# Kernel optimization log

Measured on AMD Instinct MI355X. Metric: run time of the kernel, lower is better.

## Reference

```python
import jax, jax.numpy as jnp
import numpy as np

N = 50000      # current-level nodes
N_NEXT = 2000  # next-level nodes
E = 1600000    # directed edges (before self-loops)
D_IN = 128
D_OUT = 128
LN_EPS = 1e-5


def setup_inputs() -> dict:
    key = jax.random.key(0)
    ks = jax.random.split(key, 12)
    curr_h = jax.random.normal(ks[0], (N, D_IN), dtype=jnp.float32)
    next_h = jax.random.normal(ks[1], (N_NEXT, D_IN), dtype=jnp.float32)
    inc = jax.random.uniform(ks[2], (N, N_NEXT), dtype=jnp.float32)
    src = jax.random.randint(ks[3], (E,), 0, N, dtype=jnp.int64)
    dst = jax.random.randint(ks[4], (E,), 0, N, dtype=jnp.int64)
    s = 1.0 / np.sqrt(D_IN)
    W_conv = jax.random.normal(ks[5], (D_IN, D_OUT), dtype=jnp.float32) * s
    b_conv = jnp.zeros((D_OUT,), dtype=jnp.float32)
    W_fus = jax.random.normal(ks[6], (D_IN, D_OUT), dtype=jnp.float32) * s
    b_fus = jnp.zeros((D_OUT,), dtype=jnp.float32)
    conv_w = jax.random.uniform(ks[7], (D_OUT,), dtype=jnp.float32)
    topDown_w = jax.random.uniform(ks[8], (D_OUT,), dtype=jnp.float32)
    ln_gamma = jnp.ones((D_OUT,), dtype=jnp.float32)
    ln_beta = jnp.zeros((D_OUT,), dtype=jnp.float32)
    return {
        "curr_h": curr_h, "next_h": next_h, "inc": inc,
        "src": src, "dst": dst,
        "W_conv": W_conv, "b_conv": b_conv,
        "W_fus": W_fus, "b_fus": b_fus,
        "conv_w": conv_w, "topDown_w": topDown_w,
        "ln_gamma": ln_gamma, "ln_beta": ln_beta,
    }


def _graph_conv(x, W, b, src_sl, dst_sl, norm_out, norm_in):
    # DGL GraphConv, norm='both': D_out^{-1/2} on src, sum-aggregate, D_in^{-1/2} on dst.
    h = x @ W                               # [N, D_OUT]
    h = h * norm_out[:, None]
    agg = jax.ops.segment_sum(h[src_sl], dst_sl, num_segments=N)  # SpMM
    return agg * norm_in[:, None] + b


def reference(curr_h, next_h, inc, src, dst,
              W_conv, b_conv, W_fus, b_fus,
              conv_w, topDown_w, ln_gamma, ln_beta):
    # dgl.add_self_loop
    loop = jnp.arange(N, dtype=src.dtype)
    src_sl = jnp.concatenate([src, loop])
    dst_sl = jnp.concatenate([dst, loop])
    ones = jnp.ones_like(src_sl, dtype=jnp.float32)
    out_deg = jax.ops.segment_sum(ones, src_sl, num_segments=N)
    in_deg = jax.ops.segment_sum(ones, dst_sl, num_segments=N)
    norm_out = jax.lax.rsqrt(out_deg)  # >=1 due to self-loops
    norm_in = jax.lax.rsqrt(in_deg)

    conv_layer = _graph_conv(curr_h, W_conv, b_conv, src_sl, dst_sl, norm_out, norm_in) * conv_w[None, :]
    fused_in = inc @ next_h  # dense incidence matmul [N, D_IN]
    top_down = _graph_conv(fused_in, W_fus, b_fus, src_sl, dst_sl, norm_out, norm_in) * topDown_w[None, :]

    result = conv_layer + top_down
    # LayerNorm over last dim
    mu = jnp.mean(result, axis=-1, keepdims=True)
    var = jnp.mean((result - mu) ** 2, axis=-1, keepdims=True)
    result = (result - mu) * jax.lax.rsqrt(var + LN_EPS) * ln_gamma + ln_beta
    # dropout p=0.0 (eval) -> identity; activation ReLU
    return jax.nn.relu(result)
```

## Files before the change

kernel.cpp:

```cpp
#include <hip/hip_runtime.h>
#include <hip/hip_bf16.h>

#define N_NODES   50000
#define EDGES     1600000
#define D         128
#define K_INC     2000
#define K_TOT     2128
#define K_PAD     2176
#define KTILES    34
#define LN_EPS    1e-5f

typedef float f32x4 __attribute__((ext_vector_type(4)));
typedef short short8 __attribute__((ext_vector_type(8)));
typedef ushort ushort8v __attribute__((ext_vector_type(8)));

__device__ __forceinline__ ushort f2bf(float x) {
    return __hip_bfloat16_raw(__float2bfloat16(x)).x;
}
__device__ __forceinline__ float bf_lo(uint v) { return __uint_as_float(v << 16); }
__device__ __forceinline__ float bf_hi(uint v) { return __uint_as_float(v & 0xffff0000u); }

#define GLOAD_LDS16(gp, lp) \
    __builtin_amdgcn_global_load_lds((const __attribute__((address_space(1))) void*)(gp), \
                                     (__attribute__((address_space(3))) void*)(lp), 16, 0, 0)

__global__ void probe_kernel(const int* __restrict__ src, int* __restrict__ flag) {
    __shared__ int any_nonzero;
    if (threadIdx.x == 0) any_nonzero = 0;
    __syncthreads();
    int v = src[threadIdx.x * 2 + 1];
    if (v != 0) any_nonzero = 1;
    __syncthreads();
    if (threadIdx.x == 0) flag[0] = any_nonzero ? 0 : 1;
}

__global__ void zero_kernel(int* __restrict__ p, int n) {
    int i = blockIdx.x * 256 + threadIdx.x;
    if (i < n) p[i] = 0;
}

__global__ void deg_kernel(const int* __restrict__ dst, const int* __restrict__ flag,
                           int* __restrict__ in_cnt) {
    int t = blockIdx.x * 256 + threadIdx.x;
    int e0 = t * 2;
    if (e0 >= EDGES) return;
    int d0, d1;
    if (flag[0]) {
        int4 v = *(const int4*)(dst + (size_t)e0 * 2);
        d0 = v.x; d1 = v.z;
    } else {
        int2 v = *(const int2*)(dst + e0);
        d0 = v.x; d1 = v.y;
    }
    atomicAdd(&in_cnt[d0], 1);
    atomicAdd(&in_cnt[d1], 1);
}

__global__ __launch_bounds__(1024) void scan_kernel(const int* __restrict__ cnt,
                                                    int* __restrict__ row_start) {
    __shared__ int buf[1024];
    int t = threadIdx.x;
    const int N = N_NODES;
    int chunk = (N + 1023) / 1024;
    int lo = t * chunk, hi = min(lo + chunk, N);
    int s = 0;
    for (int i = lo; i < hi; ++i) s += cnt[i];
    buf[t] = s;
    __syncthreads();
    for (int off = 1; off < 1024; off <<= 1) {
        int v = (t >= off) ? buf[t - off] : 0;
        __syncthreads();
        buf[t] += v;
        __syncthreads();
    }
    int run = (t > 0) ? buf[t - 1] : 0;
    for (int i = lo; i < hi; ++i) { row_start[i] = run; run += cnt[i]; }
    if (t == 1023) row_start[N] = buf[1023];
}

__global__ void fill_kernel(const int* __restrict__ src, const int* __restrict__ dst,
                            const int* __restrict__ flag,
                            const int* __restrict__ row_start, int* __restrict__ cursor,
                            int* __restrict__ out_deg, int* __restrict__ csr_src) {
    int t = blockIdx.x * 256 + threadIdx.x;
    int e0 = t * 2;
    if (e0 >= EDGES) return;
    int s0, s1, d0, d1;
    if (flag[0]) {
        int4 vs = *(const int4*)(src + (size_t)e0 * 2);
        int4 vd = *(const int4*)(dst + (size_t)e0 * 2);
        s0 = vs.x; s1 = vs.z; d0 = vd.x; d1 = vd.z;
    } else {
        int2 vs = *(const int2*)(src + e0);
        int2 vd = *(const int2*)(dst + e0);
        s0 = vs.x; s1 = vs.y; d0 = vd.x; d1 = vd.y;
    }
    atomicAdd(&out_deg[s0], 1);
    int p0 = atomicAdd(&cursor[d0], 1);
    csr_src[row_start[d0] + p0] = s0;
    atomicAdd(&out_deg[s1], 1);
    int p1 = atomicAdd(&cursor[d1], 1);
    csr_src[row_start[d1] + p1] = s1;
}

#define PKB 16
__global__ __launch_bounds__(128) void p_kernel(
    const float* __restrict__ next_h, const float* __restrict__ W_fus,
    const float* __restrict__ topDown_w, const float* __restrict__ W_conv,
    const float* __restrict__ conv_w, ushort* __restrict__ PbT) {
    int n = threadIdx.x;
    int k0 = blockIdx.x * PKB;
    if (k0 < K_INC) {
        float acc[PKB];
#pragma unroll
        for (int t = 0; t < PKB; ++t) acc[t] = 0.f;
        for (int j = 0; j < D; ++j) {
            float w = W_fus[(size_t)j * D + n];
#pragma unroll
            for (int t = 0; t < PKB; ++t)
                acc[t] += next_h[(size_t)(k0 + t) * D + j] * w;
        }
        float tw = topDown_w[n];
#pragma unroll
        for (int t = 0; t < PKB; ++t)
            PbT[(size_t)n * K_PAD + k0 + t] = f2bf(acc[t] * tw);
    } else if (k0 < K_TOT) {
        float cw = conv_w[n];
#pragma unroll
        for (int t = 0; t < PKB; ++t)
            PbT[(size_t)n * K_PAD + k0 + t] = f2bf(W_conv[(size_t)(k0 + t - K_INC) * D + n] * cw);
    } else {
#pragma unroll
        for (int t = 0; t < PKB; ++t)
            PbT[(size_t)n * K_PAD + k0 + t] = 0;
    }
}

__global__ __launch_bounds__(256, 3) void gemm_kernel(
    const float* __restrict__ inc, const float* __restrict__ curr_h,
    const ushort* __restrict__ PbT, const int* __restrict__ out_deg,
    ushort* __restrict__ Zs) {
    __shared__ __align__(16) ushort As[2][64][72];
    __shared__ __align__(16) ushort Bs[2][128 * 64];
    const int N = N_NODES;
    int tid = threadIdx.x;
    int wave = tid >> 6, lane = tid & 63;
    int wm = wave >> 1, wn = wave & 1;
    int r = lane & 15, q = lane >> 4;
    int rowBase = blockIdx.x * 64;

    f32x4 acc[2][4] = {};
    float4 aReg[2][2];

    auto stage_issue = [&](int kt, int nb) {
        int k0 = kt * 64;
#pragma unroll
        for (int it = 0; it < 2; ++it) {
            int u = tid + it * 256;
            int arow = u >> 3, c8 = u & 7;
            int gk = k0 + c8 * 8;
            int grow = rowBase + arow; if (grow >= N) grow = N - 1;
            if (gk < K_INC) {
                const float4* p4 = (const float4*)(inc + (size_t)grow * K_INC + gk);
                aReg[it][0] = p4[0]; aReg[it][1] = p4[1];
            } else if (gk < K_TOT) {
                const float4* p4 = (const float4*)(curr_h + (size_t)grow * D + (gk - K_INC));
                aReg[it][0] = p4[0]; aReg[it][1] = p4[1];
            } else {
                aReg[it][0] = make_float4(0.f, 0.f, 0.f, 0.f);
                aReg[it][1] = make_float4(0.f, 0.f, 0.f, 0.f);
            }
        }
#pragma unroll
        for (int it = 0; it < 4; ++it) {
            int chunk = tid + it * 256;
            int n = chunk >> 3;
            int c16 = (chunk & 7) << 4;
            int gb = c16 ^ ((n & 7) << 4);
            const char* gp = (const char*)PbT + (size_t)n * (K_PAD * 2) + (size_t)(k0 * 2) + gb;
            char* lp = (char*)(&Bs[nb][0]) + it * 4096 + wave * 1024;
            GLOAD_LDS16(gp, lp);
        }
    };
    auto stage_write = [&](int nb) {
#pragma unroll
        for (int it = 0; it < 2; ++it) {
            int u = tid + it * 256;
            int arow = u >> 3, c8 = u & 7;
            const float* f = (const float*)&aReg[it][0];
            ushort8v hv;
#pragma unroll
            for (int j = 0; j < 8; ++j) hv[j] = f2bf(f[j]);
            *(ushort8v*)&As[nb][arow][c8 * 8] = hv;
        }
    };

    stage_issue(0, 0);
    stage_write(0);
    __syncthreads();

    int cur = 0;
    for (int kt = 0; kt < KTILES; ++kt) {
        int nb = cur ^ 1;
        if (kt + 1 < KTILES) stage_issue(kt + 1, nb);
#pragma unroll
        for (int kk = 0; kk < 2; ++kk) {
            short8 af[2], bfr[4];
#pragma unroll
            for (int mi = 0; mi < 2; ++mi)
                af[mi] = *(const short8*)&As[cur][wm * 32 + mi * 16 + r][kk * 32 + q * 8];
#pragma unroll
            for (int ni = 0; ni < 4; ++ni) {
                int brow = wn * 64 + ni * 16 + r;
                int bcol = (kk * 64 + q * 16) ^ ((r & 7) << 4);
                bfr[ni] = *(const short8*)((const char*)&Bs[cur][0] + brow * 128 + bcol);
            }
#pragma unroll
            for (int mi = 0; mi < 2; ++mi)
#pragma unroll
                for (int ni = 0; ni < 4; ++ni)
                    acc[mi][ni] = __builtin_amdgcn_mfma_f32_16x16x32_bf16(af[mi], bfr[ni], acc[mi][ni], 0, 0, 0);
        }
        if (kt + 1 < KTILES) stage_write(nb);
        __syncthreads();
        cur = nb;
    }

#pragma unroll
    for (int mi = 0; mi < 2; ++mi) {
#pragma unroll
        for (int j = 0; j < 4; ++j) {
            int grow = rowBase + wm * 32 + mi * 16 + q * 4 + j;
            if (grow < N) {
                float no = rsqrtf((float)(out_deg[grow] + 1));
#pragma unroll
                for (int ni = 0; ni < 4; ++ni) {
                    int col = wn * 64 + ni * 16 + r;
                    Zs[(size_t)grow * D + col] = f2bf(acc[mi][ni][j] * no);
                }
            }
        }
    }
}

__global__ __launch_bounds__(256) void agg_ln_kernel(
    const ushort* __restrict__ Zs, const int* __restrict__ row_start,
    const int* __restrict__ csr_src,
    const float* __restrict__ b_conv, const float* __restrict__ b_fus,
    const float* __restrict__ conv_w, const float* __restrict__ topDown_w,
    const float* __restrict__ gamma, const float* __restrict__ beta,
    float* __restrict__ out) {
    int tid = threadIdx.x;
    int wid = tid >> 6, lane = tid & 63;
    int sl = lane & 15;
    int g = lane >> 4;
    int node = blockIdx.x * 16 + wid * 4 + g;
    int c0 = sl * 8;

    float a[8];
    {
        uint4 v = *(const uint4*)(Zs + (size_t)node * D + c0);
        a[0] = bf_lo(v.x); a[1] = bf_hi(v.x);
        a[2] = bf_lo(v.y); a[3] = bf_hi(v.y);
        a[4] = bf_lo(v.z); a[5] = bf_hi(v.z);
        a[6] = bf_lo(v.w); a[7] = bf_hi(v.w);
    }

    int beg = row_start[node], end = row_start[node + 1];
    int deg = end - beg;
    int m = max(deg, __shfl_xor(deg, 16));
    m = max(m, __shfl_xor(m, 32));
    int srcbase = lane & 48;

    for (int base = 0; base < m; base += 16) {
        int idx = 0;
        if (base + sl < deg) idx = csr_src[beg + base + sl];
        int cnt = deg - base;
        if (cnt >= 16) {
#pragma unroll
            for (int i = 0; i < 16; i += 4) {
                int s0 = __shfl(idx, srcbase + i);
                int s1 = __shfl(idx, srcbase + i + 1);
                int s2 = __shfl(idx, srcbase + i + 2);
                int s3 = __shfl(idx, srcbase + i + 3);
                uint4 v0 = *(const uint4*)(Zs + (size_t)s0 * D + c0);
                uint4 v1 = *(const uint4*)(Zs + (size_t)s1 * D + c0);
                uint4 v2 = *(const uint4*)(Zs + (size_t)s2 * D + c0);
                uint4 v3 = *(const uint4*)(Zs + (size_t)s3 * D + c0);
                a[0] += bf_lo(v0.x) + bf_lo(v1.x) + bf_lo(v2.x) + bf_lo(v3.x);
                a[1] += bf_hi(v0.x) + bf_hi(v1.x) + bf_hi(v2.x) + bf_hi(v3.x);
                a[2] += bf_lo(v0.y) + bf_lo(v1.y) + bf_lo(v2.y) + bf_lo(v3.y);
                a[3] += bf_hi(v0.y) + bf_hi(v1.y) + bf_hi(v2.y) + bf_hi(v3.y);
                a[4] += bf_lo(v0.z) + bf_lo(v1.z) + bf_lo(v2.z) + bf_lo(v3.z);
                a[5] += bf_hi(v0.z) + bf_hi(v1.z) + bf_hi(v2.z) + bf_hi(v3.z);
                a[6] += bf_lo(v0.w) + bf_lo(v1.w) + bf_lo(v2.w) + bf_lo(v3.w);
                a[7] += bf_hi(v0.w) + bf_hi(v1.w) + bf_hi(v2.w) + bf_hi(v3.w);
            }
        } else if (cnt > 0) {
            for (int i = 0; i < cnt; ++i) {
                int s0 = __shfl(idx, srcbase + i);
                uint4 v0 = *(const uint4*)(Zs + (size_t)s0 * D + c0);
                a[0] += bf_lo(v0.x); a[1] += bf_hi(v0.x);
                a[2] += bf_lo(v0.y); a[3] += bf_hi(v0.y);
                a[4] += bf_lo(v0.z); a[5] += bf_hi(v0.z);
                a[6] += bf_lo(v0.w); a[7] += bf_hi(v0.w);
            }
        }
    }

    float nin = rsqrtf((float)(deg + 1));
    float4 bc0 = *(const float4*)(b_conv + c0),   bc1 = *(const float4*)(b_conv + c0 + 4);
    float4 cw0 = *(const float4*)(conv_w + c0),   cw1 = *(const float4*)(conv_w + c0 + 4);
    float4 bf0 = *(const float4*)(b_fus + c0),    bf1 = *(const float4*)(b_fus + c0 + 4);
    float4 tw0 = *(const float4*)(topDown_w + c0),tw1 = *(const float4*)(topDown_w + c0 + 4);
    float bias[8] = {
        bc0.x * cw0.x + bf0.x * tw0.x, bc0.y * cw0.y + bf0.y * tw0.y,
        bc0.z * cw0.z + bf0.z * tw0.z, bc0.w * cw0.w + bf0.w * tw0.w,
        bc1.x * cw1.x + bf1.x * tw1.x, bc1.y * cw1.y + bf1.y * tw1.y,
        bc1.z * cw1.z + bf1.z * tw1.z, bc1.w * cw1.w + bf1.w * tw1.w };
    float y[8];
    float s1v = 0.f, s2v = 0.f;
#pragma unroll
    for (int j = 0; j < 8; ++j) {
        y[j] = a[j] * nin + bias[j];
        s1v += y[j]; s2v += y[j] * y[j];
    }
#pragma unroll
    for (int off = 1; off < 16; off <<= 1) {
        s1v += __shfl_xor(s1v, off);
        s2v += __shfl_xor(s2v, off);
    }
    float mu = s1v * (1.f / D);
    float var = s2v * (1.f / D) - mu * mu;
    float rstd = rsqrtf(var + LN_EPS);
    float4 ga0 = *(const float4*)(gamma + c0), ga1 = *(const float4*)(gamma + c0 + 4);
    float4 be0 = *(const float4*)(beta + c0),  be1 = *(const float4*)(beta + c0 + 4);
    float gam[8] = { ga0.x, ga0.y, ga0.z, ga0.w, ga1.x, ga1.y, ga1.z, ga1.w };
    float bet[8] = { be0.x, be0.y, be0.z, be0.w, be1.x, be1.y, be1.z, be1.w };
    float4 o0, o1;
    float r;
    r = (y[0] - mu) * rstd * gam[0] + bet[0]; o0.x = fmaxf(r, 0.f);
    r = (y[1] - mu) * rstd * gam[1] + bet[1]; o0.y = fmaxf(r, 0.f);
    r = (y[2] - mu) * rstd * gam[2] + bet[2]; o0.z = fmaxf(r, 0.f);
    r = (y[3] - mu) * rstd * gam[3] + bet[3]; o0.w = fmaxf(r, 0.f);
    r = (y[4] - mu) * rstd * gam[4] + bet[4]; o1.x = fmaxf(r, 0.f);
    r = (y[5] - mu) * rstd * gam[5] + bet[5]; o1.y = fmaxf(r, 0.f);
    r = (y[6] - mu) * rstd * gam[6] + bet[6]; o1.z = fmaxf(r, 0.f);
    r = (y[7] - mu) * rstd * gam[7] + bet[7]; o1.w = fmaxf(r, 0.f);
    *(float4*)(out + (size_t)node * D + c0) = o0;
    *(float4*)(out + (size_t)node * D + c0 + 4) = o1;
}

extern "C" void kernel_launch(void* const* d_in, const int* in_sizes, int n_in,
                              void* d_out, int out_size, void* d_ws, size_t ws_size,
                              hipStream_t stream) {
    const float* curr_h    = (const float*)d_in[0];
    const float* next_h    = (const float*)d_in[1];
    const float* inc       = (const float*)d_in[2];
    const int*   src       = (const int*)d_in[3];
    const int*   dst       = (const int*)d_in[4];
    const float* W_conv    = (const float*)d_in[5];
    const float* b_conv    = (const float*)d_in[6];
    const float* W_fus     = (const float*)d_in[7];
    const float* b_fus     = (const float*)d_in[8];
    const float* conv_w    = (const float*)d_in[9];
    const float* topDown_w = (const float*)d_in[10];
    const float* ln_gamma  = (const float*)d_in[11];
    const float* ln_beta   = (const float*)d_in[12];

    const int N = N_NODES;
    const int E = EDGES;

    char* p = (char*)d_ws;
    ushort* Zs = (ushort*)p;     p += (size_t)N * D * sizeof(ushort);
    ushort* PbT = (ushort*)p;    p += (size_t)D * K_PAD * 2;
    int* out_deg   = (int*)p;    p += (size_t)N * 4;
    int* in_cnt    = (int*)p;    p += (size_t)N * 4;
    int* cursor    = (int*)p;    p += (size_t)N * 4;
    int* row_start = (int*)p;    p += (size_t)(N + 1) * 4;
    int* idx_flag  = (int*)p;    p += 256;
    int* csr_src   = (int*)p;    p += (size_t)E * 4;

    probe_kernel<<<1, 1024, 0, stream>>>(src, idx_flag);
    zero_kernel<<<(3 * N + 255) / 256, 256, 0, stream>>>(out_deg, 3 * N);
    deg_kernel<<<(E / 2 + 255) / 256, 256, 0, stream>>>(dst, idx_flag, in_cnt);
    scan_kernel<<<1, 1024, 0, stream>>>(in_cnt, row_start);
    fill_kernel<<<(E / 2 + 255) / 256, 256, 0, stream>>>(src, dst, idx_flag, row_start,
                                                         cursor, out_deg, csr_src);
    p_kernel<<<K_PAD / PKB, 128, 0, stream>>>(next_h, W_fus, topDown_w, W_conv, conv_w, PbT);
    gemm_kernel<<<(N + 63) / 64, 256, 0, stream>>>(inc, curr_h, PbT, out_deg, Zs);
    agg_ln_kernel<<<(N + 15) / 16, 256, 0, stream>>>(Zs, row_start, csr_src,
                                                     b_conv, b_fus, conv_w, topDown_w,
                                                     ln_gamma, ln_beta, (float*)d_out);
}
```

Measured before the change: 978.5 us.

## Remap aggregation to one node per wavefront with half-wave edge split

The aggregation+LayerNorm kernel now gives each wavefront a single node instead of four nodes per wave. The two half-waves each gather alternate neighbor rows with 8-byte loads, then combine their partial sums with a cross-half shuffle. This removes idle lanes when degrees differ inside a wave and loads 64 indices per pass instead of 16. The cost is four times as many blocks, smaller per-lane loads, and half the lanes sitting idle during the epilogue and store.

```diff
diff --git a/kernel.cpp b/kernel.cpp
--- a/kernel.cpp
+++ b/kernel.cpp
@@ -250,105 +250,94 @@
     const float* __restrict__ conv_w, const float* __restrict__ topDown_w,
     const float* __restrict__ gamma, const float* __restrict__ beta,
     float* __restrict__ out) {
-    int tid = threadIdx.x;
-    int wid = tid >> 6, lane = tid & 63;
-    int sl = lane & 15;
-    int g = lane >> 4;
-    int node = blockIdx.x * 16 + wid * 4 + g;
-    int c0 = sl * 8;
-
-    float a[8];
-    {
-        uint4 v = *(const uint4*)(Zs + (size_t)node * D + c0);
-        a[0] = bf_lo(v.x); a[1] = bf_hi(v.x);
-        a[2] = bf_lo(v.y); a[3] = bf_hi(v.y);
-        a[4] = bf_lo(v.z); a[5] = bf_hi(v.z);
-        a[6] = bf_lo(v.w); a[7] = bf_hi(v.w);
+    int wid = threadIdx.x >> 6, lane = threadIdx.x & 63;
+    int node = blockIdx.x * 4 + wid;
+    if (node >= N_NODES) return;
+    int half = lane >> 5;
+    int c0 = (lane & 31) * 4;
+
+    float a0 = 0.f, a1 = 0.f, a2 = 0.f, a3 = 0.f;
+    if (!half) {
+        uint2 v = *(const uint2*)(Zs + (size_t)node * D + c0);
+        a0 = bf_lo(v.x); a1 = bf_hi(v.x); a2 = bf_lo(v.y); a3 = bf_hi(v.y);
     }
 
     int beg = row_start[node], end = row_start[node + 1];
     int deg = end - beg;
-    int m = max(deg, __shfl_xor(deg, 16));
-    m = max(m, __shfl_xor(m, 32));
-    int srcbase = lane & 48;
-
-    for (int base = 0; base < m; base += 16) {
+
+    for (int base = 0; base < deg; base += 64) {
+        int rem = deg - base;
+        int cnt = rem < 64 ? rem : 64;
         int idx = 0;
-        if (base + sl < deg) idx = csr_src[beg + base + sl];
-        int cnt = deg - base;
-        if (cnt >= 16) {
-#pragma unroll
-            for (int i = 0; i < 16; i += 4) {
-                int s0 = __shfl(idx, srcbase + i);
-                int s1 = __shfl(idx, srcbase + i + 1);
-                int s2 = __shfl(idx, srcbase + i + 2);
-                int s3 = __shfl(idx, srcbase + i + 3);
-                uint4 v0 = *(const uint4*)(Zs + (size_t)s0 * D + c0);
-                uint4 v1 = *(const uint4*)(Zs + (size_t)s1 * D + c0);
-                uint4 v2 = *(const uint4*)(Zs + (size_t)s2 * D + c0);
-                uint4 v3 = *(const uint4*)(Zs + (size_t)s3 * D + c0);
-                a[0] += bf_lo(v0.x) + bf_lo(v1.x) + bf_lo(v2.x) + bf_lo(v3.x);
-                a[1] += bf_hi(v0.x) + bf_hi(v1.x) + bf_hi(v2.x) + bf_hi(v3.x);
-                a[2] += bf_lo(v0.y) + bf_lo(v1.y) + bf_lo(v2.y) + bf_lo(v3.y);
-                a[3] += bf_hi(v0.y) + bf_hi(v1.y) + bf_hi(v2.y) + bf_hi(v3.y);
-                a[4] += bf_lo(v0.z) + bf_lo(v1.z) + bf_lo(v2.z) + bf_lo(v3.z);
-                a[5] += bf_hi(v0.z) + bf_hi(v1.z) + bf_hi(v2.z) + bf_hi(v3.z);
-                a[6] += bf_lo(v0.w) + bf_lo(v1.w) + bf_lo(v2.w) + bf_lo(v3.w);
-                a[7] += bf_hi(v0.w) + bf_hi(v1.w) + bf_hi(v2.w) + bf_hi(v3.w);
+        if (base + lane < deg) idx = csr_src[beg + base + lane];
+        int np = cnt >> 1;
+        int t = 0;
+        for (; t + 4 <= np; t += 4) {
+            int s0 = __shfl(idx, 2 * t + half);
+            int s1 = __shfl(idx, 2 * t + 2 + half);
+            int s2 = __shfl(idx, 2 * t + 4 + half);
+            int s3 = __shfl(idx, 2 * t + 6 + half);
+            uint2 v0 = *(const uint2*)(Zs + (size_t)s0 * D + c0);
+            uint2 v1 = *(const uint2*)(Zs + (size_t)s1 * D + c0);
+            uint2 v2 = *(const uint2*)(Zs + (size_t)s2 * D + c0);
+            uint2 v3 = *(const uint2*)(Zs + (size_t)s3 * D + c0);
+            a0 += bf_lo(v0.x) + bf_lo(v1.x) + bf_lo(v2.x) + bf_lo(v3.x);
+            a1 += bf_hi(v0.x) + bf_hi(v1.x) + bf_hi(v2.x) + bf_hi(v3.x);
+            a2 += bf_lo(v0.y) + bf_lo(v1.y) + bf_lo(v2.y) + bf_lo(v3.y);
+            a3 += bf_hi(v0.y) + bf_hi(v1.y) + bf_hi(v2.y) + bf_hi(v3.y);
+        }
+        for (; t < np; ++t) {
+            int s0 = __shfl(idx, 2 * t + half);
+            uint2 v0 = *(const uint2*)(Zs + (size_t)s0 * D + c0);
+            a0 += bf_lo(v0.x); a1 += bf_hi(v0.x);
+            a2 += bf_lo(v0.y); a3 += bf_hi(v0.y);
+        }
+        if (cnt & 1) {
+            int s0 = __shfl(idx, cnt - 1);
+            if (!half) {
+                uint2 v0 = *(const uint2*)(Zs + (size_t)s0 * D + c0);
+                a0 += bf_lo(v0.x); a1 += bf_hi(v0.x);
+                a2 += bf_lo(v0.y); a3 += bf_hi(v0.y);
             }
-        } else if (cnt > 0) {
-            for (int i = 0; i < cnt; ++i) {
-                int s0 = __shfl(idx, srcbase + i);
-                uint4 v0 = *(const uint4*)(Zs + (size_t)s0 * D + c0);
-                a[0] += bf_lo(v0.x); a[1] += bf_hi(v0.x);
-                a[2] += bf_lo(v0.y); a[3] += bf_hi(v0.y);
-                a[4] += bf_lo(v0.z); a[5] += bf_hi(v0.z);
-                a[6] += bf_lo(v0.w); a[7] += bf_hi(v0.w);
-            }
-        }
-    }
+        }
+    }
+
+    a0 += __shfl_xor(a0, 32);
+    a1 += __shfl_xor(a1, 32);
+    a2 += __shfl_xor(a2, 32);
+    a3 += __shfl_xor(a3, 32);
 
     float nin = rsqrtf((float)(deg + 1));
-    float4 bc0 = *(const float4*)(b_conv + c0),   bc1 = *(const float4*)(b_conv + c0 + 4);
-    float4 cw0 = *(const float4*)(conv_w + c0),   cw1 = *(const float4*)(conv_w + c0 + 4);
-    float4 bf0 = *(const float4*)(b_fus + c0),    bf1 = *(const float4*)(b_fus + c0 + 4);
-    float4 tw0 = *(const float4*)(topDown_w + c0),tw1 = *(const float4*)(topDown_w + c0 + 4);
-    float bias[8] = {
-        bc0.x * cw0.x + bf0.x * tw0.x, bc0.y * cw0.y + bf0.y * tw0.y,
-        bc0.z * cw0.z + bf0.z * tw0.z, bc0.w * cw0.w + bf0.w * tw0.w,
-        bc1.x * cw1.x + bf1.x * tw1.x, bc1.y * cw1.y + bf1.y * tw1.y,
-        bc1.z * cw1.z + bf1.z * tw1.z, bc1.w * cw1.w + bf1.w * tw1.w };
-    float y[8];
-    float s1v = 0.f, s2v = 0.f;
-#pragma unroll
-    for (int j = 0; j < 8; ++j) {
-        y[j] = a[j] * nin + bias[j];
-        s1v += y[j]; s2v += y[j] * y[j];
-    }
-#pragma unroll
-    for (int off = 1; off < 16; off <<= 1) {
+    float4 bc = *(const float4*)(b_conv + c0);
+    float4 cw = *(const float4*)(conv_w + c0);
+    float4 bfv = *(const float4*)(b_fus + c0);
+    float4 tw = *(const float4*)(topDown_w + c0);
+    float y0 = a0 * nin + bc.x * cw.x + bfv.x * tw.x;
+    float y1 = a1 * nin + bc.y * cw.y + bfv.y * tw.y;
+    float y2 = a2 * nin + bc.z * cw.z + bfv.z * tw.z;
+    float y3 = a3 * nin + bc.w * cw.w + bfv.w * tw.w;
+
+    float s1v = y0 + y1 + y2 + y3;
+    float s2v = y0 * y0 + y1 * y1 + y2 * y2 + y3 * y3;
+#pragma unroll
+    for (int off = 1; off < 32; off <<= 1) {
         s1v += __shfl_xor(s1v, off);
         s2v += __shfl_xor(s2v, off);
     }
     float mu = s1v * (1.f / D);
     float var = s2v * (1.f / D) - mu * mu;
     float rstd = rsqrtf(var + LN_EPS);
-    float4 ga0 = *(const float4*)(gamma + c0), ga1 = *(const float4*)(gamma + c0 + 4);
-    float4 be0 = *(const float4*)(beta + c0),  be1 = *(const float4*)(beta + c0 + 4);
-    float gam[8] = { ga0.x, ga0.y, ga0.z, ga0.w, ga1.x, ga1.y, ga1.z, ga1.w };
-    float bet[8] = { be0.x, be0.y, be0.z, be0.w, be1.x, be1.y, be1.z, be1.w };
-    float4 o0, o1;
-    float r;
-    r = (y[0] - mu) * rstd * gam[0] + bet[0]; o0.x = fmaxf(r, 0.f);
-    r = (y[1] - mu) * rstd * gam[1] + bet[1]; o0.y = fmaxf(r, 0.f);
-    r = (y[2] - mu) * rstd * gam[2] + bet[2]; o0.z = fmaxf(r, 0.f);
-    r = (y[3] - mu) * rstd * gam[3] + bet[3]; o0.w = fmaxf(r, 0.f);
-    r = (y[4] - mu) * rstd * gam[4] + bet[4]; o1.x = fmaxf(r, 0.f);
-    r = (y[5] - mu) * rstd * gam[5] + bet[5]; o1.y = fmaxf(r, 0.f);
-    r = (y[6] - mu) * rstd * gam[6] + bet[6]; o1.z = fmaxf(r, 0.f);
-    r = (y[7] - mu) * rstd * gam[7] + bet[7]; o1.w = fmaxf(r, 0.f);
-    *(float4*)(out + (size_t)node * D + c0) = o0;
-    *(float4*)(out + (size_t)node * D + c0 + 4) = o1;
+    if (!half) {
+        float4 ga = *(const float4*)(gamma + c0);
+        float4 be = *(const float4*)(beta + c0);
+        float4 o;
+        float r;
+        r = (y0 - mu) * rstd * ga.x + be.x; o.x = fmaxf(r, 0.f);
+        r = (y1 - mu) * rstd * ga.y + be.y; o.y = fmaxf(r, 0.f);
+        r = (y2 - mu) * rstd * ga.z + be.z; o.z = fmaxf(r, 0.f);
+        r = (y3 - mu) * rstd * ga.w + be.w; o.w = fmaxf(r, 0.f);
+        *(float4*)(out + (size_t)node * D + c0) = o;
+    }
 }
 
 extern "C" void kernel_launch(void* const* d_in, const int* in_sizes, int n_in,
@@ -389,7 +378,7 @@
                                                          cursor, out_deg, csr_src);
     p_kernel<<<K_PAD / PKB, 128, 0, stream>>>(next_h, W_fus, topDown_w, W_conv, conv_w, PbT);
     gemm_kernel<<<(N + 63) / 64, 256, 0, stream>>>(inc, curr_h, PbT, out_deg, Zs);
-    agg_ln_kernel<<<(N + 15) / 16, 256, 0, stream>>>(Zs, row_start, csr_src,
-                                                     b_conv, b_fus, conv_w, topDown_w,
-                                                     ln_gamma, ln_beta, (float*)d_out);
-}
+    agg_ln_kernel<<<(N + 3) / 4, 256, 0, stream>>>(Zs, row_start, csr_src,
+                                                   b_conv, b_fus, conv_w, topDown_w,
+                                                   ln_gamma, ln_beta, (float*)d_out);
+}
```

Result: no change. 961.4 us (-1.8%).
